# Performance work log

Measured on AMD Instinct MI355X. Metric: run time of the kernel, lower is better.

## Reference

```python
import jax, jax.numpy as jnp
import numpy as np

N_NODES = 50000
EMBED_DIM = 128
N_EDGES = 500000


def setup_inputs() -> dict:
    key = jax.random.key(0)
    k_x, k_e, k_w1, k_w2 = jax.random.split(key, 4)
    s = 1.0 / np.sqrt(EMBED_DIM)
    return {
        "x": jax.random.normal(k_x, (N_NODES, EMBED_DIM), dtype=jnp.float32),
        "edge_index": jax.random.randint(k_e, (2, N_EDGES), 0, N_NODES, dtype=jnp.int64),
        "W1": jax.random.normal(k_w1, (EMBED_DIM, EMBED_DIM), dtype=jnp.float32) * s,
        "b1": jnp.zeros((EMBED_DIM,), dtype=jnp.float32),
        "W2": jax.random.normal(k_w2, (EMBED_DIM, EMBED_DIM), dtype=jnp.float32) * s,
        "b2": jnp.zeros((EMBED_DIM,), dtype=jnp.float32),
    }


def _gcn_conv(x, src, dst, norm, W, b, n_nodes):
    # PyG GCNConv: h = x @ W; out[i] = sum_{j->i} norm_e * h[j] + b
    h = x @ W                              # [N, D] small GEMM
    msg = h[src] * norm[:, None]           # gather + scale, [E+N, D]
    out = jax.ops.segment_sum(msg, dst, num_segments=n_nodes)
    return out + b


def reference(x, edge_index, W1, b1, W2, b2):
    n = x.shape[0]
    # add self loops (GCNConv default add_self_loops=True)
    loop = jnp.arange(n, dtype=edge_index.dtype)
    src = jnp.concatenate([edge_index[0], loop])
    dst = jnp.concatenate([edge_index[1], loop])
    # symmetric normalization: deg over destination (in-degree incl. self loop)
    deg = jax.ops.segment_sum(jnp.ones_like(src, dtype=x.dtype), dst, num_segments=n)
    dis = jnp.where(deg > 0, jax.lax.rsqrt(jnp.maximum(deg, 1e-12)), 0.0)
    norm = dis[src] * dis[dst]             # [E+N]

    init_embeds = x  # Identity init embedding
    h = jnp.tanh(_gcn_conv(init_embeds, src, dst, norm, W1, b1, n))
    h = jnp.tanh(_gcn_conv(h, src, dst, norm, W2, b2, n))
    return (h, init_embeds)
```

## Files before the change

### kernel.cpp

```cpp
#include <hip/hip_runtime.h>

#define D 128
#define CAP 64

typedef short bf16x8 __attribute__((ext_vector_type(8)));
typedef float f32x4  __attribute__((ext_vector_type(4)));
typedef float f32x2  __attribute__((ext_vector_type(2)));

__device__ __forceinline__ unsigned f2bf(float f) {
    unsigned u = __float_as_uint(f);
    return (u + 0x7fffu + ((u >> 16) & 1u)) >> 16;
}

__global__ __launch_bounds__(256) void k_pre(
    const float4* __restrict__ x4, float4* __restrict__ out2,
    const float* __restrict__ W1, const float* __restrict__ W2,
    ushort* __restrict__ Wt1, ushort* __restrict__ Wt2,
    const int* __restrict__ ei, int* __restrict__ cnt, ushort* __restrict__ ewsrc,
    uint* __restrict__ Xf8, uint* __restrict__ H1f8,
    int n4, int ne, int cb, int nsent) {
    const int blk = blockIdx.x, t = threadIdx.x;
    if (blk < cb) {
        int e = blk * 256 + t;
        if (e < ne) {
            int s = ei[e];
            int d = ei[ne + e];
            int slot = atomicAdd(&cnt[d], 1);
            if (slot < CAP - 1) ewsrc[(uint)d * CAP + slot] = (ushort)s;
        }
    } else if (blk < cb + 128) {
        if (blk == cb) {
            if (t < 32) Xf8[(size_t)nsent * 32 + t] = 0;
            else if (t < 64) H1f8[(size_t)nsent * 32 + (t - 32)] = 0;
        }
        int i = (blk - cb) * 256 + t;
        const float* W = (i < 16384) ? W1 : W2;
        ushort* Wt = (i < 16384) ? Wt1 : Wt2;
        int j = i & 16383;
        int nn = j >> 7, k = j & 127;
        Wt[nn * 128 + k] = (ushort)f2bf(W[k * 128 + nn]);
    } else {
        int i = (blk - cb - 128) * 256 + t;
        if (i < n4) out2[i] = x4[i];
    }
}

__global__ __launch_bounds__(256) void k_scale(
    const float4* __restrict__ x4, const int* __restrict__ cnt,
    uint* __restrict__ Xf8, int n4) {
    int i = blockIdx.x * 256 + threadIdx.x;
    if (i >= n4) return;
    float s = rsqrtf((float)cnt[i >> 5] + 1.0f);
    float4 v = x4[i];
    uint q = __builtin_amdgcn_cvt_pk_fp8_f32(v.x * s, v.y * s, 0, false);
    q = __builtin_amdgcn_cvt_pk_fp8_f32(v.z * s, v.w * s, q, true);
    Xf8[i] = q;
}

template <bool FP8OUT>
__global__ __launch_bounds__(256) void k_layer(
    const int* __restrict__ cnt, ushort* __restrict__ ewsrc,
    const uint* __restrict__ Ain8, const ushort* __restrict__ Wt,
    const float* __restrict__ bias, void* __restrict__ out, int n, int nsent) {
    __shared__ ushort atile[16 * 136];
    __shared__ float otile[16 * 132];
    const int wid = threadIdx.x >> 6;
    const int lane = threadIdx.x & 63;
    const int base = blockIdx.x * 16;

    {
        const int ln = threadIdx.x >> 4;
        const int k = threadIdx.x & 15;
        const int node = base + ln;
        if (node < n && k < 4) {
            int deg = cnt[node]; if (deg > CAP - 1) deg = CAP - 1;
            int pdeg = (deg + 4) & ~3;
            int p = deg + k;
            if (p < pdeg) ewsrc[(uint)node * CAP + p] = (ushort)((k == 0) ? node : nsent);
        }
    }
    __syncthreads();

    const int fl = lane & 31;
    const int half = lane >> 5;

#pragma unroll
    for (int j = 0; j < 4; ++j) {
        const int node = base + wid * 4 + j;
        float a0 = 0.f, a1 = 0.f, a2 = 0.f, a3 = 0.f;
        float di = 1.f;
        if (node < n) {
            int degc = cnt[node];
            di = rsqrtf((float)degc + 1.0f);
            if (degc > CAP - 1) degc = CAP - 1;
            const int pdeg = (degc + 4) & ~3;
            const ushort* rs = ewsrc + (uint)node * CAP;
            int e = 0;
            for (; e + 8 <= pdeg; e += 8) {
                uint4 q = *(const uint4*)(rs + e);
                uint r0 = half ? (q.x >> 16) : (q.x & 0xffffu);
                uint r1 = half ? (q.y >> 16) : (q.y & 0xffffu);
                uint r2 = half ? (q.z >> 16) : (q.z & 0xffffu);
                uint r3 = half ? (q.w >> 16) : (q.w & 0xffffu);
                uint u0 = Ain8[r0 * 32 + fl];
                uint u1 = Ain8[r1 * 32 + fl];
                uint u2 = Ain8[r2 * 32 + fl];
                uint u3 = Ain8[r3 * 32 + fl];
                f32x2 l0 = __builtin_amdgcn_cvt_pk_f32_fp8(u0, false);
                f32x2 h0 = __builtin_amdgcn_cvt_pk_f32_fp8(u0, true);
                f32x2 l1 = __builtin_amdgcn_cvt_pk_f32_fp8(u1, false);
                f32x2 h1 = __builtin_amdgcn_cvt_pk_f32_fp8(u1, true);
                f32x2 l2 = __builtin_amdgcn_cvt_pk_f32_fp8(u2, false);
                f32x2 h2 = __builtin_amdgcn_cvt_pk_f32_fp8(u2, true);
                f32x2 l3 = __builtin_amdgcn_cvt_pk_f32_fp8(u3, false);
                f32x2 h3 = __builtin_amdgcn_cvt_pk_f32_fp8(u3, true);
                a0 += l0.x + l1.x + l2.x + l3.x;
                a1 += l0.y + l1.y + l2.y + l3.y;
                a2 += h0.x + h1.x + h2.x + h3.x;
                a3 += h0.y + h1.y + h2.y + h3.y;
            }
            if (e < pdeg) {
                uint2 q = *(const uint2*)(rs + e);
                uint r0 = half ? (q.x >> 16) : (q.x & 0xffffu);
                uint r1 = half ? (q.y >> 16) : (q.y & 0xffffu);
                uint u0 = Ain8[r0 * 32 + fl];
                uint u1 = Ain8[r1 * 32 + fl];
                f32x2 l0 = __builtin_amdgcn_cvt_pk_f32_fp8(u0, false);
                f32x2 h0 = __builtin_amdgcn_cvt_pk_f32_fp8(u0, true);
                f32x2 l1 = __builtin_amdgcn_cvt_pk_f32_fp8(u1, false);
                f32x2 h1 = __builtin_amdgcn_cvt_pk_f32_fp8(u1, true);
                a0 += l0.x + l1.x;
                a1 += l0.y + l1.y;
                a2 += h0.x + h1.x;
                a3 += h0.y + h1.y;
            }
        }
        a0 += __shfl_xor(a0, 32, 64);
        a1 += __shfl_xor(a1, 32, 64);
        a2 += __shfl_xor(a2, 32, 64);
        a3 += __shfl_xor(a3, 32, 64);
        if (half == 0) {
            a0 *= di; a1 *= di; a2 *= di; a3 *= di;
            uint p0 = f2bf(a0) | (f2bf(a1) << 16);
            uint p1 = f2bf(a2) | (f2bf(a3) << 16);
            uint* arow = (uint*)atile + (wid * 4 + j) * 68;
            arow[2 * fl] = p0;
            arow[2 * fl + 1] = p1;
        }
    }
    __syncthreads();

    const int m = lane & 15, quad = lane >> 4;
    const ushort* arow = atile + m * 136 + quad * 8;
    bf16x8 afr[4];
#pragma unroll
    for (int kc = 0; kc < 4; ++kc) afr[kc] = *(const bf16x8*)(arow + kc * 32);

    f32x4 acc[2];
#pragma unroll
    for (int t2 = 0; t2 < 2; ++t2) {
        acc[t2] = (f32x4){0.f, 0.f, 0.f, 0.f};
        const int t = wid * 2 + t2;
        const ushort* wrow = Wt + (size_t)(t * 16 + m) * 128 + quad * 8;
#pragma unroll
        for (int kc = 0; kc < 4; ++kc) {
            bf16x8 b = *(const bf16x8*)(wrow + kc * 32);
            acc[t2] = __builtin_amdgcn_mfma_f32_16x16x32_bf16(afr[kc], b, acc[t2], 0, 0, 0);
        }
    }

#pragma unroll
    for (int t2 = 0; t2 < 2; ++t2) {
        const int t = wid * 2 + t2;
        float bb = bias[t * 16 + m];
#pragma unroll
        for (int r = 0; r < 4; ++r)
            otile[(quad * 4 + r) * 132 + t * 16 + m] = tanhf(acc[t2][r] + bb);
    }
    __syncthreads();

    const int row = threadIdx.x >> 4, seg = threadIdx.x & 15;
    if (base + row < n) {
        const float* src = &otile[row * 132 + seg * 8];
        if (FP8OUT) {
            float s = rsqrtf((float)cnt[base + row] + 1.0f);
            uint q0 = __builtin_amdgcn_cvt_pk_fp8_f32(src[0] * s, src[1] * s, 0, false);
            q0 = __builtin_amdgcn_cvt_pk_fp8_f32(src[2] * s, src[3] * s, q0, true);
            uint q1 = __builtin_amdgcn_cvt_pk_fp8_f32(src[4] * s, src[5] * s, 0, false);
            q1 = __builtin_amdgcn_cvt_pk_fp8_f32(src[6] * s, src[7] * s, q1, true);
            ((uint2*)out)[(size_t)(base + row) * 16 + seg] = make_uint2(q0, q1);
        } else {
            float4* dst = (float4*)((float*)out + (size_t)(base + row) * 128 + seg * 8);
            dst[0] = *(const float4*)(src);
            dst[1] = *(const float4*)(src + 4);
        }
    }
}

extern "C" void kernel_launch(void* const* d_in, const int* in_sizes, int n_in,
                              void* d_out, int out_size, void* d_ws, size_t ws_size,
                              hipStream_t stream) {
    const float* x  = (const float*)d_in[0];
    const int*   ei = (const int*)d_in[1];
    const float* W1 = (const float*)d_in[2];
    const float* b1 = (const float*)d_in[3];
    const float* W2 = (const float*)d_in[4];
    const float* b2 = (const float*)d_in[5];
    const int N = in_sizes[0] / D;
    const int E = in_sizes[1] / 2;
    float* out = (float*)d_out;

    char* ws = (char*)d_ws;
    const size_t KB = 1024, MB = 1024 * KB;
    int*    cnt   = (int*)(ws + 0);
    ushort* ewsrc = (ushort*)(ws + 1 * MB);
    uint*   Xf8   = (uint*)(ws + 8 * MB);
    uint*   H1f8  = (uint*)(ws + 16 * MB);
    ushort* Wt1   = (ushort*)(ws + 24 * MB);
    ushort* Wt2   = (ushort*)(ws + 24 * MB + 64 * KB);

    const int n4 = N * D / 4;
    const int nb = (n4 + 255) / 256;
    const int cb = (E + 255) / 256;
    const int lblocks = (N + 15) / 16;

    hipMemsetAsync(cnt, 0, (size_t)(N + 1) * sizeof(int), stream);
    k_pre<<<cb + 128 + nb, 256, 0, stream>>>(
        (const float4*)x, (float4*)(out + (size_t)N * D),
        W1, W2, Wt1, Wt2, ei, cnt, ewsrc, Xf8, H1f8, n4, E, cb, N);
    k_scale<<<nb, 256, 0, stream>>>((const float4*)x, cnt, Xf8, n4);

    k_layer<true><<<lblocks, 256, 0, stream>>>(cnt, ewsrc, Xf8, Wt1,
                                               b1, (void*)H1f8, N, N);
    k_layer<false><<<lblocks, 256, 0, stream>>>(cnt, ewsrc, H1f8, Wt2,
                                                b2, (void*)out, N, N);
}
```

Baseline: 191.1 us.

## Fuse all stages into one persistent cooperative kernel with grid syncs

Merges the preprocessing, scaling and both GCN layer kernels into one cooperative persistent kernel that uses grid-wide syncs between phases. Layer tiles are processed in a grid-stride loop, and the gather loop now interleaves four nodes per wave with sentinel padding to raise memory-level parallelism. The aim is to remove kernel launch gaps and per-kernel tails. In exchange the grid is capped at about 1024 blocks, there are three grid barriers, and the atomics-based CSR build runs with fewer threads.

```diff
diff --git a/kernel.cpp b/kernel.cpp
--- a/kernel.cpp
+++ b/kernel.cpp
@@ -1,4 +1,7 @@
 #include <hip/hip_runtime.h>
+#include <hip/hip_cooperative_groups.h>
+
+namespace cg = cooperative_groups;
 
 #define D 128
 #define CAP 64
@@ -12,203 +15,205 @@
     return (u + 0x7fffu + ((u >> 16) & 1u)) >> 16;
 }
 
-__global__ __launch_bounds__(256) void k_pre(
-    const float4* __restrict__ x4, float4* __restrict__ out2,
-    const float* __restrict__ W1, const float* __restrict__ W2,
+template <bool FP8OUT>
+__device__ __forceinline__ void layer_tiles(
+    const int* __restrict__ cnt, const ushort* __restrict__ ewsrc,
+    const uint* __restrict__ Ain8, const ushort* __restrict__ Wt,
+    const float* __restrict__ bias, void* __restrict__ out,
+    int n, int nsent, int ntiles, ushort* atile, float* otile) {
+    const int wid = threadIdx.x >> 6;
+    const int lane = threadIdx.x & 63;
+    const int fl = lane & 31;
+    const int half = lane >> 5;
+    const uint sentw = ((uint)nsent) | (((uint)nsent) << 16);
+
+    for (int tile = blockIdx.x; tile < ntiles; tile += gridDim.x) {
+        __syncthreads();
+        const int base = tile * 16;
+
+        int nd[4], pdeg[4]; float di[4]; int maxp = 0;
+#pragma unroll
+        for (int j = 0; j < 4; ++j) {
+            int node = base + wid * 4 + j;
+            bool ok = node < n;
+            int dg = ok ? cnt[node] : 0;
+            di[j] = __builtin_amdgcn_rsqf((float)dg + 1.0f);
+            if (dg > CAP - 1) dg = CAP - 1;
+            nd[j] = ok ? node : nsent;
+            pdeg[j] = ok ? ((dg + 4) & ~3) : 0;
+            maxp = max(maxp, pdeg[j]);
+        }
+        float a0[4] = {0,0,0,0}, a1[4] = {0,0,0,0};
+        float a2[4] = {0,0,0,0}, a3[4] = {0,0,0,0};
+
+        for (int e = 0; e < maxp; e += 8) {
+            uint uu[16];
+#pragma unroll
+            for (int j = 0; j < 4; ++j) {
+                const ushort* rs = ewsrc + (uint)nd[j] * CAP + e;
+                uint2 qa = *(const uint2*)(rs);
+                uint2 qb = *(const uint2*)(rs + 4);
+                if (e + 4 > pdeg[j]) { qa.x = sentw; qa.y = sentw; }
+                if (e + 8 > pdeg[j]) { qb.x = sentw; qb.y = sentw; }
+                uint r0 = half ? (qa.x >> 16) : (qa.x & 0xffffu);
+                uint r1 = half ? (qa.y >> 16) : (qa.y & 0xffffu);
+                uint r2 = half ? (qb.x >> 16) : (qb.x & 0xffffu);
+                uint r3 = half ? (qb.y >> 16) : (qb.y & 0xffffu);
+                uu[j * 4 + 0] = Ain8[r0 * 32 + fl];
+                uu[j * 4 + 1] = Ain8[r1 * 32 + fl];
+                uu[j * 4 + 2] = Ain8[r2 * 32 + fl];
+                uu[j * 4 + 3] = Ain8[r3 * 32 + fl];
+            }
+#pragma unroll
+            for (int j = 0; j < 4; ++j) {
+                f32x2 l0 = __builtin_amdgcn_cvt_pk_f32_fp8(uu[j * 4 + 0], false);
+                f32x2 h0 = __builtin_amdgcn_cvt_pk_f32_fp8(uu[j * 4 + 0], true);
+                f32x2 l1 = __builtin_amdgcn_cvt_pk_f32_fp8(uu[j * 4 + 1], false);
+                f32x2 h1 = __builtin_amdgcn_cvt_pk_f32_fp8(uu[j * 4 + 1], true);
+                f32x2 l2 = __builtin_amdgcn_cvt_pk_f32_fp8(uu[j * 4 + 2], false);
+                f32x2 h2 = __builtin_amdgcn_cvt_pk_f32_fp8(uu[j * 4 + 2], true);
+                f32x2 l3 = __builtin_amdgcn_cvt_pk_f32_fp8(uu[j * 4 + 3], false);
+                f32x2 h3 = __builtin_amdgcn_cvt_pk_f32_fp8(uu[j * 4 + 3], true);
+                a0[j] += l0.x + l1.x + l2.x + l3.x;
+                a1[j] += l0.y + l1.y + l2.y + l3.y;
+                a2[j] += h0.x + h1.x + h2.x + h3.x;
+                a3[j] += h0.y + h1.y + h2.y + h3.y;
+            }
+        }
+#pragma unroll
+        for (int j = 0; j < 4; ++j) {
+            float s0 = a0[j] + __shfl_xor(a0[j], 32, 64);
+            float s1 = a1[j] + __shfl_xor(a1[j], 32, 64);
+            float s2 = a2[j] + __shfl_xor(a2[j], 32, 64);
+            float s3 = a3[j] + __shfl_xor(a3[j], 32, 64);
+            if (half == 0) {
+                s0 *= di[j]; s1 *= di[j]; s2 *= di[j]; s3 *= di[j];
+                uint p0 = f2bf(s0) | (f2bf(s1) << 16);
+                uint p1 = f2bf(s2) | (f2bf(s3) << 16);
+                uint* arow = (uint*)atile + (wid * 4 + j) * 68;
+                arow[2 * fl] = p0;
+                arow[2 * fl + 1] = p1;
+            }
+        }
+        __syncthreads();
+
+        const int m = lane & 15, quad = lane >> 4;
+        const ushort* ar = atile + m * 136 + quad * 8;
+        bf16x8 afr[4];
+#pragma unroll
+        for (int kc = 0; kc < 4; ++kc) afr[kc] = *(const bf16x8*)(ar + kc * 32);
+
+        f32x4 acc[2];
+#pragma unroll
+        for (int t2 = 0; t2 < 2; ++t2) {
+            acc[t2] = (f32x4){0.f, 0.f, 0.f, 0.f};
+            const int t = wid * 2 + t2;
+            const ushort* wrow = Wt + (size_t)(t * 16 + m) * 128 + quad * 8;
+#pragma unroll
+            for (int kc = 0; kc < 4; ++kc) {
+                bf16x8 b = *(const bf16x8*)(wrow + kc * 32);
+                acc[t2] = __builtin_amdgcn_mfma_f32_16x16x32_bf16(afr[kc], b, acc[t2], 0, 0, 0);
+            }
+        }
+
+#pragma unroll
+        for (int t2 = 0; t2 < 2; ++t2) {
+            const int t = wid * 2 + t2;
+            float bb = bias[t * 16 + m];
+#pragma unroll
+            for (int r = 0; r < 4; ++r)
+                otile[(quad * 4 + r) * 132 + t * 16 + m] = tanhf(acc[t2][r] + bb);
+        }
+        __syncthreads();
+
+        const int row = threadIdx.x >> 4, seg = threadIdx.x & 15;
+        if (base + row < n) {
+            const float* src = &otile[row * 132 + seg * 8];
+            if (FP8OUT) {
+                float s = rsqrtf((float)cnt[base + row] + 1.0f);
+                uint q0 = __builtin_amdgcn_cvt_pk_fp8_f32(src[0] * s, src[1] * s, 0, false);
+                q0 = __builtin_amdgcn_cvt_pk_fp8_f32(src[2] * s, src[3] * s, q0, true);
+                uint q1 = __builtin_amdgcn_cvt_pk_fp8_f32(src[4] * s, src[5] * s, 0, false);
+                q1 = __builtin_amdgcn_cvt_pk_fp8_f32(src[6] * s, src[7] * s, q1, true);
+                ((uint2*)out)[(size_t)(base + row) * 16 + seg] = make_uint2(q0, q1);
+            } else {
+                float4* dst = (float4*)((float*)out + (size_t)(base + row) * 128 + seg * 8);
+                dst[0] = *(const float4*)(src);
+                dst[1] = *(const float4*)(src + 4);
+            }
+        }
+    }
+}
+
+__global__ __launch_bounds__(256, 4) void k_all(
+    const float4* __restrict__ x4, float4* __restrict__ out2, float* __restrict__ out1,
+    const float* __restrict__ W1, const float* __restrict__ b1,
+    const float* __restrict__ W2, const float* __restrict__ b2,
     ushort* __restrict__ Wt1, ushort* __restrict__ Wt2,
     const int* __restrict__ ei, int* __restrict__ cnt, ushort* __restrict__ ewsrc,
     uint* __restrict__ Xf8, uint* __restrict__ H1f8,
-    int n4, int ne, int cb, int nsent) {
-    const int blk = blockIdx.x, t = threadIdx.x;
-    if (blk < cb) {
-        int e = blk * 256 + t;
-        if (e < ne) {
-            int s = ei[e];
-            int d = ei[ne + e];
-            int slot = atomicAdd(&cnt[d], 1);
-            if (slot < CAP - 1) ewsrc[(uint)d * CAP + slot] = (ushort)s;
-        }
-    } else if (blk < cb + 128) {
-        if (blk == cb) {
-            if (t < 32) Xf8[(size_t)nsent * 32 + t] = 0;
-            else if (t < 64) H1f8[(size_t)nsent * 32 + (t - 32)] = 0;
-        }
-        int i = (blk - cb) * 256 + t;
-        const float* W = (i < 16384) ? W1 : W2;
-        ushort* Wt = (i < 16384) ? Wt1 : Wt2;
-        int j = i & 16383;
+    int N, int E, int n4) {
+    cg::grid_group grid = cg::this_grid();
+    __shared__ ushort atile[16 * 136];
+    __shared__ float otile[16 * 132];
+    const int tid = blockIdx.x * blockDim.x + threadIdx.x;
+    const int nth = gridDim.x * blockDim.x;
+    const int nsent = N;
+
+    for (int e = tid; e < E; e += nth) {
+        int s = ei[e], d = ei[E + e];
+        int sl = atomicAdd(&cnt[d], 1);
+        if (sl < CAP - 1) ewsrc[(uint)d * CAP + sl] = (ushort)s;
+    }
+    for (int i = tid; i < 2 * D * D; i += nth) {
+        const float* W = (i < D * D) ? W1 : W2;
+        ushort* Wt = (i < D * D) ? Wt1 : Wt2;
+        int j = i & (D * D - 1);
         int nn = j >> 7, k = j & 127;
         Wt[nn * 128 + k] = (ushort)f2bf(W[k * 128 + nn]);
-    } else {
-        int i = (blk - cb - 128) * 256 + t;
-        if (i < n4) out2[i] = x4[i];
-    }
-}
-
-__global__ __launch_bounds__(256) void k_scale(
-    const float4* __restrict__ x4, const int* __restrict__ cnt,
-    uint* __restrict__ Xf8, int n4) {
-    int i = blockIdx.x * 256 + threadIdx.x;
-    if (i >= n4) return;
-    float s = rsqrtf((float)cnt[i >> 5] + 1.0f);
-    float4 v = x4[i];
-    uint q = __builtin_amdgcn_cvt_pk_fp8_f32(v.x * s, v.y * s, 0, false);
-    q = __builtin_amdgcn_cvt_pk_fp8_f32(v.z * s, v.w * s, q, true);
-    Xf8[i] = q;
-}
-
-template <bool FP8OUT>
-__global__ __launch_bounds__(256) void k_layer(
-    const int* __restrict__ cnt, ushort* __restrict__ ewsrc,
-    const uint* __restrict__ Ain8, const ushort* __restrict__ Wt,
-    const float* __restrict__ bias, void* __restrict__ out, int n, int nsent) {
-    __shared__ ushort atile[16 * 136];
-    __shared__ float otile[16 * 132];
-    const int wid = threadIdx.x >> 6;
-    const int lane = threadIdx.x & 63;
-    const int base = blockIdx.x * 16;
-
-    {
-        const int ln = threadIdx.x >> 4;
-        const int k = threadIdx.x & 15;
-        const int node = base + ln;
-        if (node < n && k < 4) {
-            int deg = cnt[node]; if (deg > CAP - 1) deg = CAP - 1;
-            int pdeg = (deg + 4) & ~3;
-            int p = deg + k;
-            if (p < pdeg) ewsrc[(uint)node * CAP + p] = (ushort)((k == 0) ? node : nsent);
-        }
-    }
-    __syncthreads();
-
-    const int fl = lane & 31;
-    const int half = lane >> 5;
-
-#pragma unroll
-    for (int j = 0; j < 4; ++j) {
-        const int node = base + wid * 4 + j;
-        float a0 = 0.f, a1 = 0.f, a2 = 0.f, a3 = 0.f;
-        float di = 1.f;
-        if (node < n) {
-            int degc = cnt[node];
-            di = rsqrtf((float)degc + 1.0f);
-            if (degc > CAP - 1) degc = CAP - 1;
-            const int pdeg = (degc + 4) & ~3;
-            const ushort* rs = ewsrc + (uint)node * CAP;
-            int e = 0;
-            for (; e + 8 <= pdeg; e += 8) {
-                uint4 q = *(const uint4*)(rs + e);
-                uint r0 = half ? (q.x >> 16) : (q.x & 0xffffu);
-                uint r1 = half ? (q.y >> 16) : (q.y & 0xffffu);
-                uint r2 = half ? (q.z >> 16) : (q.z & 0xffffu);
-                uint r3 = half ? (q.w >> 16) : (q.w & 0xffffu);
-                uint u0 = Ain8[r0 * 32 + fl];
-                uint u1 = Ain8[r1 * 32 + fl];
-                uint u2 = Ain8[r2 * 32 + fl];
-                uint u3 = Ain8[r3 * 32 + fl];
-                f32x2 l0 = __builtin_amdgcn_cvt_pk_f32_fp8(u0, false);
-                f32x2 h0 = __builtin_amdgcn_cvt_pk_f32_fp8(u0, true);
-                f32x2 l1 = __builtin_amdgcn_cvt_pk_f32_fp8(u1, false);
-                f32x2 h1 = __builtin_amdgcn_cvt_pk_f32_fp8(u1, true);
-                f32x2 l2 = __builtin_amdgcn_cvt_pk_f32_fp8(u2, false);
-                f32x2 h2 = __builtin_amdgcn_cvt_pk_f32_fp8(u2, true);
-                f32x2 l3 = __builtin_amdgcn_cvt_pk_f32_fp8(u3, false);
-                f32x2 h3 = __builtin_amdgcn_cvt_pk_f32_fp8(u3, true);
-                a0 += l0.x + l1.x + l2.x + l3.x;
-                a1 += l0.y + l1.y + l2.y + l3.y;
-                a2 += h0.x + h1.x + h2.x + h3.x;
-                a3 += h0.y + h1.y + h2.y + h3.y;
-            }
-            if (e < pdeg) {
-                uint2 q = *(const uint2*)(rs + e);
-                uint r0 = half ? (q.x >> 16) : (q.x & 0xffffu);
-                uint r1 = half ? (q.y >> 16) : (q.y & 0xffffu);
-                uint u0 = Ain8[r0 * 32 + fl];
-                uint u1 = Ain8[r1 * 32 + fl];
-                f32x2 l0 = __builtin_amdgcn_cvt_pk_f32_fp8(u0, false);
-                f32x2 h0 = __builtin_amdgcn_cvt_pk_f32_fp8(u0, true);
-                f32x2 l1 = __builtin_amdgcn_cvt_pk_f32_fp8(u1, false);
-                f32x2 h1 = __builtin_amdgcn_cvt_pk_f32_fp8(u1, true);
-                a0 += l0.x + l1.x;
-                a1 += l0.y + l1.y;
-                a2 += h0.x + h1.x;
-                a3 += h0.y + h1.y;
-            }
-        }
-        a0 += __shfl_xor(a0, 32, 64);
-        a1 += __shfl_xor(a1, 32, 64);
-        a2 += __shfl_xor(a2, 32, 64);
-        a3 += __shfl_xor(a3, 32, 64);
-        if (half == 0) {
-            a0 *= di; a1 *= di; a2 *= di; a3 *= di;
-            uint p0 = f2bf(a0) | (f2bf(a1) << 16);
-            uint p1 = f2bf(a2) | (f2bf(a3) << 16);
-            uint* arow = (uint*)atile + (wid * 4 + j) * 68;
-            arow[2 * fl] = p0;
-            arow[2 * fl + 1] = p1;
-        }
-    }
-    __syncthreads();
-
-    const int m = lane & 15, quad = lane >> 4;
-    const ushort* arow = atile + m * 136 + quad * 8;
-    bf16x8 afr[4];
-#pragma unroll
-    for (int kc = 0; kc < 4; ++kc) afr[kc] = *(const bf16x8*)(arow + kc * 32);
-
-    f32x4 acc[2];
-#pragma unroll
-    for (int t2 = 0; t2 < 2; ++t2) {
-        acc[t2] = (f32x4){0.f, 0.f, 0.f, 0.f};
-        const int t = wid * 2 + t2;
-        const ushort* wrow = Wt + (size_t)(t * 16 + m) * 128 + quad * 8;
-#pragma unroll
-        for (int kc = 0; kc < 4; ++kc) {
-            bf16x8 b = *(const bf16x8*)(wrow + kc * 32);
-            acc[t2] = __builtin_amdgcn_mfma_f32_16x16x32_bf16(afr[kc], b, acc[t2], 0, 0, 0);
-        }
-    }
-
-#pragma unroll
-    for (int t2 = 0; t2 < 2; ++t2) {
-        const int t = wid * 2 + t2;
-        float bb = bias[t * 16 + m];
-#pragma unroll
-        for (int r = 0; r < 4; ++r)
-            otile[(quad * 4 + r) * 132 + t * 16 + m] = tanhf(acc[t2][r] + bb);
-    }
-    __syncthreads();
-
-    const int row = threadIdx.x >> 4, seg = threadIdx.x & 15;
-    if (base + row < n) {
-        const float* src = &otile[row * 132 + seg * 8];
-        if (FP8OUT) {
-            float s = rsqrtf((float)cnt[base + row] + 1.0f);
-            uint q0 = __builtin_amdgcn_cvt_pk_fp8_f32(src[0] * s, src[1] * s, 0, false);
-            q0 = __builtin_amdgcn_cvt_pk_fp8_f32(src[2] * s, src[3] * s, q0, true);
-            uint q1 = __builtin_amdgcn_cvt_pk_fp8_f32(src[4] * s, src[5] * s, 0, false);
-            q1 = __builtin_amdgcn_cvt_pk_fp8_f32(src[6] * s, src[7] * s, q1, true);
-            ((uint2*)out)[(size_t)(base + row) * 16 + seg] = make_uint2(q0, q1);
-        } else {
-            float4* dst = (float4*)((float*)out + (size_t)(base + row) * 128 + seg * 8);
-            dst[0] = *(const float4*)(src);
-            dst[1] = *(const float4*)(src + 4);
-        }
-    }
+    }
+    for (int i = tid; i < n4; i += nth) out2[i] = x4[i];
+    __threadfence();
+    grid.sync();
+
+    for (int i = tid; i < n4; i += nth) {
+        float s = rsqrtf((float)cnt[i >> 5] + 1.0f);
+        float4 v = x4[i];
+        uint q = __builtin_amdgcn_cvt_pk_fp8_f32(v.x * s, v.y * s, 0, false);
+        q = __builtin_amdgcn_cvt_pk_fp8_f32(v.z * s, v.w * s, q, true);
+        Xf8[i] = q;
+    }
+    for (int v = tid; v < N; v += nth) {
+        int dg = cnt[v]; if (dg > CAP - 1) dg = CAP - 1;
+        int pd = (dg + 4) & ~3;
+        ushort* r = ewsrc + (uint)v * CAP;
+        r[dg] = (ushort)v;
+        for (int p = dg + 1; p < pd; ++p) r[p] = (ushort)nsent;
+    }
+    __threadfence();
+    grid.sync();
+
+    const int ntiles = (N + 15) >> 4;
+    layer_tiles<true>(cnt, ewsrc, Xf8, Wt1, b1, (void*)H1f8, N, nsent, ntiles, atile, otile);
+    __threadfence();
+    grid.sync();
+
+    layer_tiles<false>(cnt, ewsrc, H1f8, Wt2, b2, (void*)out1, N, nsent, ntiles, atile, otile);
 }
 
 extern "C" void kernel_launch(void* const* d_in, const int* in_sizes, int n_in,
                               void* d_out, int out_size, void* d_ws, size_t ws_size,
                               hipStream_t stream) {
-    const float* x  = (const float*)d_in[0];
+    const float4* x4 = (const float4*)d_in[0];
     const int*   ei = (const int*)d_in[1];
     const float* W1 = (const float*)d_in[2];
     const float* b1 = (const float*)d_in[3];
     const float* W2 = (const float*)d_in[4];
     const float* b2 = (const float*)d_in[5];
-    const int N = in_sizes[0] / D;
-    const int E = in_sizes[1] / 2;
-    float* out = (float*)d_out;
+    int N = in_sizes[0] / D;
+    int E = in_sizes[1] / 2;
+    float* out1 = (float*)d_out;
+    float4* out2 = (float4*)(out1 + (size_t)N * D);
 
     char* ws = (char*)d_ws;
     const size_t KB = 1024, MB = 1024 * KB;
@@ -219,19 +224,28 @@
     ushort* Wt1   = (ushort*)(ws + 24 * MB);
     ushort* Wt2   = (ushort*)(ws + 24 * MB + 64 * KB);
 
-    const int n4 = N * D / 4;
-    const int nb = (n4 + 255) / 256;
-    const int cb = (E + 255) / 256;
-    const int lblocks = (N + 15) / 16;
+    int n4 = N * D / 4;
 
     hipMemsetAsync(cnt, 0, (size_t)(N + 1) * sizeof(int), stream);
-    k_pre<<<cb + 128 + nb, 256, 0, stream>>>(
-        (const float4*)x, (float4*)(out + (size_t)N * D),
-        W1, W2, Wt1, Wt2, ei, cnt, ewsrc, Xf8, H1f8, n4, E, cb, N);
-    k_scale<<<nb, 256, 0, stream>>>((const float4*)x, cnt, Xf8, n4);
-
-    k_layer<true><<<lblocks, 256, 0, stream>>>(cnt, ewsrc, Xf8, Wt1,
-                                               b1, (void*)H1f8, N, N);
-    k_layer<false><<<lblocks, 256, 0, stream>>>(cnt, ewsrc, H1f8, Wt2,
-                                                b2, (void*)out, N, N);
-}
+    hipMemsetAsync(Xf8 + (size_t)N * 32, 0, 128, stream);
+    hipMemsetAsync(H1f8 + (size_t)N * 32, 0, 128, stream);
+
+    static int g_grid = 0;
+    if (g_grid == 0) {
+        int bpc = 0;
+        hipOccupancyMaxActiveBlocksPerMultiprocessor(&bpc, k_all, 256, 0);
+        if (bpc < 1) bpc = 1;
+        g_grid = bpc * 256;
+        if (g_grid > 1024) g_grid = 1024;
+    }
+
+    void* args[] = {
+        (void*)&x4, (void*)&out2, (void*)&out1,
+        (void*)&W1, (void*)&b1, (void*)&W2, (void*)&b2,
+        (void*)&Wt1, (void*)&Wt2,
+        (void*)&ei, (void*)&cnt, (void*)&ewsrc,
+        (void*)&Xf8, (void*)&H1f8,
+        (void*)&N, (void*)&E, (void*)&n4,
+    };
+    hipLaunchCooperativeKernel((const void*)k_all, dim3(g_grid), dim3(256), args, 0, stream);
+}
```

After: 587.3 us. +207.3%, slower.
